# Kernel optimization log

Measured on AMD Instinct MI355X. Metric: run time of the kernel, lower is better.

The kernel has to match this reference:

```python
import jax, jax.numpy as jnp
import numpy as np

B, L, W = 128, 8192, 31

def setup_inputs() -> dict:
    key = jax.random.key(0)
    x = jax.random.normal(key, (B, L), dtype=jnp.float32)
    return {"x": x, "win_size": W}

def reference(x, win_size):
    # Sliding-window unfold: out[b, i, j] = x[b, i + j] for i in [0, L-2r), j in [0, win_size)
    r = win_size // 2
    L_ = x.shape[1]
    n_win = L_ - 2 * r  # number of window-center positions
    idx = jnp.arange(n_win)[:, None] + jnp.arange(win_size)[None, :]  # [n_win, W]
    return x[:, idx]  # [B, n_win, W]
```

## Files before the change

kernel.cpp:

```cpp
#include <hip/hip_runtime.h>


constexpr int B_   = 128;
constexpr int L_   = 8192;
constexpr int W_   = 31;
constexpr int NWIN = L_ - (W_ - 1);
constexpr int PERB = NWIN * W_;
constexpr int N2   = PERB / 2;
constexpr int BLOCK = 256;
constexpr int K     = 8;
constexpr int BLOCKS_X = (N2 + BLOCK * K - 1) / (BLOCK * K);

typedef float f32x2 __attribute__((ext_vector_type(2)));

__global__ __launch_bounds__(BLOCK) void unfold_kernel(const float* __restrict__ x,
                                                       float* __restrict__ out) {
    const int b = blockIdx.y;
    const float* __restrict__ xb = x + b * L_;
    f32x2* __restrict__ ob = reinterpret_cast<f32x2*>(out) + (size_t)b * N2;

    unsigned t2 = blockIdx.x * (BLOCK * K) + threadIdx.x;
    unsigned q  = 2u * t2;
    unsigned i  = q / 31u;
    unsigned j  = q - 31u * i;

#pragma unroll
    for (int s = 0; s < K; ++s) {
        if (t2 < (unsigned)N2) {
            unsigned in0 = i + j;
            unsigned in1 = in0 + 1u - (j == 30u ? 30u : 0u);
            f32x2 v;
            v.x = xb[in0];
            v.y = xb[in1];
            __builtin_nontemporal_store(v, &ob[t2]);
        }
        t2 += BLOCK;
        i  += 16u;
        j  += 16u;
        if (j >= 31u) { j -= 31u; ++i; }
    }
}

extern "C" void kernel_launch(void* const* d_in, const int* in_sizes, int n_in,
                              void* d_out, int out_size, void* d_ws, size_t ws_size,
                              hipStream_t stream) {
    const float* x = (const float*)d_in[0];
    float* out = (float*)d_out;
    dim3 grid(BLOCKS_X, B_);
    unfold_kernel<<<grid, BLOCK, 0, stream>>>(x, out);
}
```

Measured before the change: 159.7 us.

## Flatten batch into 1D grid and write float4 vectors across batch boundaries

Flattens the output over batch and window positions into a single index space so each thread can write 16-byte float4 vectors, which the per-batch layout could not guarantee because each batch holds an odd number of floats. Each vector may cross a batch boundary, so a conditional reads from the next batch row. The nontemporal store is replaced by a plain store and the per-thread unroll drops from 8 to 4. This adds index bookkeeping and per-element branches in exchange for wider stores.

After: 146.4 us. 1.09x faster.

```diff
diff --git a/kernel.cpp b/kernel.cpp
--- a/kernel.cpp
+++ b/kernel.cpp
@@ -6,38 +6,56 @@
 constexpr int W_   = 31;
 constexpr int NWIN = L_ - (W_ - 1);
 constexpr int PERB = NWIN * W_;
-constexpr int N2   = PERB / 2;
+constexpr long long TOTAL = (long long)B_ * PERB;
+constexpr int NVEC  = (int)(TOTAL / 4);
 constexpr int BLOCK = 256;
-constexpr int K     = 8;
-constexpr int BLOCKS_X = (N2 + BLOCK * K - 1) / (BLOCK * K);
+constexpr int K     = 4;
+constexpr int CHUNK = BLOCK * K;
+constexpr int GRID  = (NVEC + CHUNK - 1) / CHUNK;
 
-typedef float f32x2 __attribute__((ext_vector_type(2)));
+typedef float f32x4 __attribute__((ext_vector_type(4)));
 
 __global__ __launch_bounds__(BLOCK) void unfold_kernel(const float* __restrict__ x,
                                                        float* __restrict__ out) {
-    const int b = blockIdx.y;
+    unsigned t = blockIdx.x * CHUNK + threadIdx.x;
+    unsigned o = t << 2;
+    unsigned b = o / (unsigned)PERB;
+    unsigned q = o - b * (unsigned)PERB;
+    unsigned i = q / 31u;
+    unsigned j = q - 31u * i;
     const float* __restrict__ xb = x + b * L_;
-    f32x2* __restrict__ ob = reinterpret_cast<f32x2*>(out) + (size_t)b * N2;
-
-    unsigned t2 = blockIdx.x * (BLOCK * K) + threadIdx.x;
-    unsigned q  = 2u * t2;
-    unsigned i  = q / 31u;
-    unsigned j  = q - 31u * i;
+    f32x4* __restrict__ o4 = reinterpret_cast<f32x4*>(out);
 
 #pragma unroll
     for (int s = 0; s < K; ++s) {
-        if (t2 < (unsigned)N2) {
-            unsigned in0 = i + j;
-            unsigned in1 = in0 + 1u - (j == 30u ? 30u : 0u);
-            f32x2 v;
-            v.x = xb[in0];
-            v.y = xb[in1];
-            __builtin_nontemporal_store(v, &ob[t2]);
+        if (t < (unsigned)NVEC) {
+            f32x4 v;
+            unsigned base = i + j;
+#pragma unroll
+            for (int k = 0; k < 4; ++k) {
+                unsigned jk  = j + (unsigned)k;
+                unsigned idx = base + (unsigned)k - (jk >= 31u ? 30u : 0u);
+                float val;
+                if (q + (unsigned)k >= (unsigned)PERB) {
+                    val = xb[L_ + (q + (unsigned)k - (unsigned)PERB)];
+                } else {
+                    val = xb[idx];
+                }
+                v[k] = val;
+            }
+            o4[t] = v;
         }
-        t2 += BLOCK;
-        i  += 16u;
-        j  += 16u;
+        t += BLOCK;
+        q += 1024u;
+        i += 33u;
+        j += 1u;
         if (j >= 31u) { j -= 31u; ++i; }
+        if (q >= (unsigned)PERB) {
+            q -= (unsigned)PERB;
+            xb += L_;
+            i = q / 31u;
+            j = q - 31u * i;
+        }
     }
 }
 
@@ -46,6 +64,5 @@
                               hipStream_t stream) {
     const float* x = (const float*)d_in[0];
     float* out = (float*)d_out;
-    dim3 grid(BLOCKS_X, B_);
-    unfold_kernel<<<grid, BLOCK, 0, stream>>>(x, out);
+    unfold_kernel<<<GRID, BLOCK, 0, stream>>>(x, out);
 }
```
